# Performance work log

Hardware: AMD Instinct MI355X
Metric: run time of the kernel (lower is better)

The kernel has to match this reference:

```python
import jax, jax.numpy as jnp
import numpy as np

N_HEADS = 16


def setup_inputs() -> dict:
    key = jax.random.key(0)
    k1, k2, k3 = jax.random.split(key, 3)
    B, T, C = 4, 2048, 1024
    x = jax.random.normal(k1, (B, T, C), dtype=jnp.float32)
    # torch nn.Linear weights are (out_features, in_features); y = x @ W.T
    w_in = jax.random.normal(k2, (3 * C, C), dtype=jnp.float32) * 0.02
    w_out = jax.random.normal(k3, (C, C), dtype=jnp.float32) * 0.02
    return {"x": x, "w_in": w_in, "w_out": w_out}


def reference(x, w_in, w_out):
    B, T, C = x.shape
    H = N_HEADS
    hd = C // H

    qkv = x @ w_in.T                      # [B, T, 3C]
    q, k, v = jnp.split(qkv, 3, axis=2)   # each [B, T, C]

    def heads(t):
        return t.reshape(B, T, H, hd).transpose(0, 2, 1, 3)  # [B, H, T, hd]

    q, k, v = heads(q), heads(k), heads(v)

    scale = 1.0 / jnp.sqrt(jnp.float32(hd))
    scores = jnp.einsum('bhqd,bhkd->bhqk', q, k) * scale      # [B, H, T, T]
    causal = jnp.tril(jnp.ones((T, T), dtype=bool))
    scores = jnp.where(causal, scores, -jnp.inf)
    attn = jax.nn.softmax(scores, axis=-1)
    y = jnp.einsum('bhqk,bhkd->bhqd', attn, v)                # [B, H, T, hd]
    y = y.transpose(0, 2, 1, 3).reshape(B, T, C)
    return y @ w_out.T
```

## Files before the change

### kernel.cpp

```cpp
#include <hip/hip_runtime.h>
#include <stdint.h>

#define BB 4
#define TT 2048
#define CC 1024
#define HH 16
#define HD 64
#define C3 3072
#define MM (BB*TT)

typedef __bf16 bf16_t;
typedef bf16_t bf16x8 __attribute__((ext_vector_type(8)));
typedef float f32x4 __attribute__((ext_vector_type(4)));
typedef unsigned short u16;
typedef u16 u16x8 __attribute__((ext_vector_type(8)));
typedef uint32_t u32;

static __device__ __forceinline__ u16 f2bf(float f){
  u32 u = __builtin_bit_cast(u32, f);
  u32 r = (u + 0x7fffu + ((u >> 16) & 1u)) >> 16;
  return (u16)r;
}

static __device__ __forceinline__ f32x4 mfma16(bf16x8 a, bf16x8 b, f32x4 c){
  return __builtin_amdgcn_mfma_f32_16x16x32_bf16(a, b, c, 0, 0, 0);
}

typedef __attribute__((address_space(1))) void* gas_t;
typedef __attribute__((address_space(3))) void* las_t;
static __device__ __forceinline__ void gload16(const void* g, void* l){
  __builtin_amdgcn_global_load_lds((gas_t)g, (las_t)l, 16, 0, 0);
}

__global__ __launch_bounds__(256) void cvt_bf16(const float* __restrict__ in,
                                                u16* __restrict__ out, int n8){
  int stride = gridDim.x * blockDim.x;
  for (int i = blockIdx.x * blockDim.x + threadIdx.x; i < n8; i += stride){
    const float4* p = (const float4*)in + (size_t)i * 2;
    float4 a = p[0], b = p[1];
    u16x8 o;
    o[0]=f2bf(a.x); o[1]=f2bf(a.y); o[2]=f2bf(a.z); o[3]=f2bf(a.w);
    o[4]=f2bf(b.x); o[5]=f2bf(b.y); o[6]=f2bf(b.z); o[7]=f2bf(b.w);
    *((u16x8*)out + i) = o;
  }
}

template<int OUTBF>
__global__ __launch_bounds__(256) void gemm_bt(const u16* __restrict__ A,
                                               const u16* __restrict__ Bm,
                                               void* __restrict__ Cp,
                                               int M, int N, int K,
                                               int nbx, int cpx){
  __shared__ u16 As[128*64];
  __shared__ u16 Bs[128*64];
  const int bid = blockIdx.x;
  const int nb = (bid & 7) * cpx + (bid >> 3);
  const int by = nb / nbx, bx = nb - by * nbx;
  const int tid  = threadIdx.x;
  const int lane = tid & 63;
  const int w    = tid >> 6;
  const int m0   = by * 128;
  const int n0   = bx * 128;
  const int wm   = (w >> 1) * 64;
  const int wn   = (w & 1) * 64;
  const int lr   = lane & 15;
  const int lg4  = lane >> 4;

  f32x4 acc[4][4] = {};

  const int rq  = tid >> 3;
  const int c8s = ((tid & 7) ^ (rq & 7)) * 8;
  const u16* gA = A  + (size_t)(m0 + rq) * K + c8s;
  const u16* gB = Bm + (size_t)(n0 + rq) * K + c8s;
  char* lA = (char*)As + tid*16;
  char* lB = (char*)Bs + tid*16;

  for (int k0 = 0; k0 < K; k0 += 64){
    #pragma unroll
    for (int q = 0; q < 4; q++){
      gload16(gA + (size_t)(q*32)*K + k0, lA + q*4096);
      gload16(gB + (size_t)(q*32)*K + k0, lB + q*4096);
    }
    __syncthreads();
    #pragma unroll
    for (int kk = 0; kk < 2; kk++){
      bf16x8 af[4], bfr[4];
      #pragma unroll
      for (int m = 0; m < 4; m++){
        int row = wm + m*16 + lr;
        int slot = ((kk<<2) | lg4) ^ (row & 7);
        af[m] = *(const bf16x8*)((const char*)As + row*128 + slot*16);
      }
      #pragma unroll
      for (int n = 0; n < 4; n++){
        int row = wn + n*16 + lr;
        int slot = ((kk<<2) | lg4) ^ (row & 7);
        bfr[n] = *(const bf16x8*)((const char*)Bs + row*128 + slot*16);
      }
      #pragma unroll
      for (int m = 0; m < 4; m++)
        #pragma unroll
        for (int n = 0; n < 4; n++)
          acc[m][n] = mfma16(af[m], bfr[n], acc[m][n]);
    }
    __syncthreads();
  }

  const int cr = lg4 * 4;
  #pragma unroll
  for (int m = 0; m < 4; m++)
    #pragma unroll
    for (int n = 0; n < 4; n++)
      #pragma unroll
      for (int j = 0; j < 4; j++){
        size_t row = (size_t)(m0 + wm + m*16 + cr + j);
        size_t col = (size_t)(n0 + wn + n*16 + lr);
        if (OUTBF) ((u16*)Cp)[row*(size_t)N + col] = f2bf(acc[m][n][j]);
        else       ((float*)Cp)[row*(size_t)N + col] = acc[m][n][j];
      }
}

__global__ __launch_bounds__(256, 3) void attn_fwd(const u16* __restrict__ qkv,
                                                   u16* __restrict__ y){
  __shared__ u16 Kl[64*72];
  __shared__ u16 Vt[64*72];
  const int bid = blockIdx.x;
  const int tq = bid >> 6;
  const int h = bid & 15, b = (bid >> 4) & 3;
  const int tid = threadIdx.x, lane = tid & 63, w = tid >> 6;
  const int lr = lane & 15, lg = lane >> 4;
  const size_t base = (size_t)b * TT * C3;
  const int qA = tq*64 + w*16;
  const int qB = (31-tq)*64 + w*16;
  const float SC = 0.18033688011112042f;

  bf16x8 qf[2][2];
  {
    const u16* qp0 = qkv + base + (size_t)(qA + lr) * C3 + h*HD;
    qf[0][0] = *(const bf16x8*)(qp0 + lg*8);
    qf[0][1] = *(const bf16x8*)(qp0 + 32 + lg*8);
    const u16* qp1 = qkv + base + (size_t)(qB + lr) * C3 + h*HD;
    qf[1][0] = *(const bf16x8*)(qp1 + lg*8);
    qf[1][1] = *(const bf16x8*)(qp1 + 32 + lg*8);
    #pragma unroll
    for (int m = 0; m < 2; m++)
      #pragma unroll
      for (int i = 0; i < 2; i++)
        #pragma unroll
        for (int e = 0; e < 8; e++)
          qf[m][i][e] = (bf16_t)((float)qf[m][i][e] * SC);
  }

  const int rK = tid >> 3, cK = tid & 7;
  const int rV = tid & 31, cV = tid >> 5;
  const u16* gK = qkv + base + (size_t)rK * C3 + CC   + h*HD + cK*8;
  const u16* gV = qkv + base + (size_t)rV * C3 + 2*CC + h*HD + cV*8;

  const int kkey = ((rK >> 3) & 1) << 5;
  const int kw0 = rK*72 + ((cK*8) ^ kkey);
  const int kw1 = (rK+32)*72 + ((cK*8) ^ kkey);

  const int rdx = ((lr >> 2) & 1) << 5;
  const int rbase = 8*(lr >> 2) + (lr & 3);

  u16x8 kreg[2], vreg[2];
  kreg[0] = *(const u16x8*)(gK);
  kreg[1] = *(const u16x8*)(gK + (size_t)32*C3);
  vreg[0] = *(const u16x8*)(gV);
  vreg[1] = *(const u16x8*)(gV + (size_t)32*C3);

  f32x4 o[2][4] = {};
  float mj[2] = {-1e30f, -1e30f};
  float lj[2] = {0.f, 0.f};

  const int ktmax = 31 - tq;
  for (int kt = 0; kt <= ktmax; kt++){
    __syncthreads();
    *(u16x8*)&Kl[kw0] = kreg[0];
    *(u16x8*)&Kl[kw1] = kreg[1];
    #pragma unroll
    for (int i = 0; i < 2; i++)
      #pragma unroll
      for (int e = 0; e < 8; e++)
        Vt[(cV*8+e)*72 + i*32 + rV] = vreg[i][e];
    __syncthreads();

    if (kt < ktmax){
      const u16* gk2 = gK + (size_t)(kt+1)*64*C3;
      const u16* gv2 = gV + (size_t)(kt+1)*64*C3;
      kreg[0] = *(const u16x8*)(gk2);
      kreg[1] = *(const u16x8*)(gk2 + (size_t)32*C3);
      vreg[0] = *(const u16x8*)(gv2);
      vreg[1] = *(const u16x8*)(gv2 + (size_t)32*C3);
    }

    const bool m0act = (kt <= tq);

    f32x4 s[2][4] = {};
    __builtin_amdgcn_s_setprio(1);
    #pragma unroll
    for (int n = 0; n < 4; n++){
      const int rho = 32*(n>>1) + 4*(n&1) + rbase;
      bf16x8 kb0 = *(const bf16x8*)&Kl[rho*72 + ((     lg*8) ^ rdx)];
      bf16x8 kb1 = *(const bf16x8*)&Kl[rho*72 + ((32 + lg*8) ^ rdx)];
      if (m0act){
        s[0][n] = mfma16(kb0, qf[0][0], s[0][n]);
        s[0][n] = mfma16(kb1, qf[0][1], s[0][n]);
      }
      s[1][n] = mfma16(kb0, qf[1][0], s[1][n]);
      s[1][n] = mfma16(kb1, qf[1][1], s[1][n]);
    }
    __builtin_amdgcn_s_setprio(0);

    bf16x8 paA[2], paB[2];
    #pragma unroll
    for (int m = 0; m < 2; m++){
      if (m == 0 && !m0act) continue;
      const int qrow = (m ? qB : qA) + lr;
      const bool dm = (kt == (m ? ktmax : tq));
      if (dm){
        #pragma unroll
        for (int n = 0; n < 4; n++)
          #pragma unroll
          for (int j = 0; j < 4; j++)
            if (kt*64 + 32*(n>>1) + 8*lg + 4*(n&1) + j > qrow)
              s[m][n][j] = -1e30f;
      }
      float tm = s[m][0][0];
      #pragma unroll
      for (int n = 0; n < 4; n++)
        #pragma unroll
        for (int j = 0; j < 4; j++) tm = fmaxf(tm, s[m][n][j]);
      tm = fmaxf(tm, __shfl_xor(tm, 16, 64));
      tm = fmaxf(tm, __shfl_xor(tm, 32, 64));
      float mo = mj[m];
      if (!__all(tm <= mo + 4.0f)){
        float mn = fmaxf(mo, tm);
        float al = __builtin_amdgcn_exp2f(mo - mn);
        mj[m] = mn;
        lj[m] *= al;
        float a0 = __shfl(al, lg*4+0, 16);
        float a1 = __shfl(al, lg*4+1, 16);
        float a2 = __shfl(al, lg*4+2, 16);
        float a3 = __shfl(al, lg*4+3, 16);
        #pragma unroll
        for (int n = 0; n < 4; n++){
          o[m][n][0] *= a0; o[m][n][1] *= a1;
          o[m][n][2] *= a2; o[m][n][3] *= a3;
        }
      }
      float mm = mj[m];
      float ps = 0.f;
      bf16x8 pa, pb;
      #pragma unroll
      for (int n = 0; n < 4; n++){
        float p0 = __builtin_amdgcn_exp2f(s[m][n][0] - mm);
        float p1 = __builtin_amdgcn_exp2f(s[m][n][1] - mm);
        float p2 = __builtin_amdgcn_exp2f(s[m][n][2] - mm);
        float p3 = __builtin_amdgcn_exp2f(s[m][n][3] - mm);
        ps += (p0 + p1) + (p2 + p3);
        if (n == 0){ pa[0]=(bf16_t)p0; pa[1]=(bf16_t)p1; pa[2]=(bf16_t)p2; pa[3]=(bf16_t)p3; }
        if (n == 1){ pa[4]=(bf16_t)p0; pa[5]=(bf16_t)p1; pa[6]=(bf16_t)p2; pa[7]=(bf16_t)p3; }
        if (n == 2){ pb[0]=(bf16_t)p0; pb[1]=(bf16_t)p1; pb[2]=(bf16_t)p2; pb[3]=(bf16_t)p3; }
        if (n == 3){ pb[4]=(bf16_t)p0; pb[5]=(bf16_t)p1; pb[6]=(bf16_t)p2; pb[7]=(bf16_t)p3; }
      }
      ps += __shfl_xor(ps, 16, 64);
      ps += __shfl_xor(ps, 32, 64);
      lj[m] += ps;
      paA[m] = pa; paB[m] = pb;
    }

    __builtin_amdgcn_s_setprio(1);
    #pragma unroll
    for (int n = 0; n < 4; n++){
      bf16x8 vb0 = *(const bf16x8*)&Vt[(n*16+lr)*72 +      lg*8];
      bf16x8 vb1 = *(const bf16x8*)&Vt[(n*16+lr)*72 + 32 + lg*8];
      if (m0act){
        o[0][n] = mfma16(paA[0], vb0, o[0][n]);
        o[0][n] = mfma16(paB[0], vb1, o[0][n]);
      }
      o[1][n] = mfma16(paA[1], vb0, o[1][n]);
      o[1][n] = mfma16(paB[1], vb1, o[1][n]);
    }
    __builtin_amdgcn_s_setprio(0);
  }

  #pragma unroll
  for (int m = 0; m < 2; m++){
    float inv = 1.0f / lj[m];
    float i0 = __shfl(inv, lg*4+0, 16);
    float i1 = __shfl(inv, lg*4+1, 16);
    float i2 = __shfl(inv, lg*4+2, 16);
    float i3 = __shfl(inv, lg*4+3, 16);
    const int qb = (m ? qB : qA);
    #pragma unroll
    for (int j = 0; j < 4; j++){
      float ij = (j==0) ? i0 : (j==1) ? i1 : (j==2) ? i2 : i3;
      size_t row = (size_t)b*TT + qb + lg*4 + j;
      #pragma unroll
      for (int n = 0; n < 4; n++)
        y[row*CC + h*HD + n*16 + lr] = f2bf(o[m][n][j] * ij);
    }
  }
}

extern "C" void kernel_launch(void* const* d_in, const int* in_sizes, int n_in,
                              void* d_out, int out_size, void* d_ws, size_t ws_size,
                              hipStream_t stream){
  const float* x     = (const float*)d_in[0];
  const float* w_in  = (const float*)d_in[1];
  const float* w_out = (const float*)d_in[2];
  float* out = (float*)d_out;

  u16* xb   = (u16*)d_ws;
  u16* wib  = xb  + (size_t)MM * CC;
  u16* wob  = wib + (size_t)C3 * CC;
  u16* qkvb = wob + (size_t)CC * CC;
  u16* yb   = xb;

  auto nblk = [](int n8){ int g = (n8 + 255) / 256; return g > 2048 ? 2048 : g; };
  cvt_bf16<<<nblk(MM*CC/8), 256, 0, stream>>>(x,     xb,  MM*CC/8);
  cvt_bf16<<<nblk(C3*CC/8), 256, 0, stream>>>(w_in,  wib, C3*CC/8);
  cvt_bf16<<<nblk(CC*CC/8), 256, 0, stream>>>(w_out, wob, CC*CC/8);

  gemm_bt<1><<<1536, 256, 0, stream>>>(xb, wib, (void*)qkvb, MM, C3, CC, 24, 192);
  attn_fwd<<<1024, 256, 0, stream>>>(qkvb, yb);
  gemm_bt<0><<<512, 256, 0, stream>>>(yb, wob, (void*)out, MM, CC, CC, 8, 64);
}
```

Before: 172.7 us.

## Double-buffer K/V LDS tiles and pack V transpose stores into 32-bit writes

Shared-memory K and V tiles are now double-buffered by iteration parity, so the leading __syncthreads per iteration is dropped and only one barrier per key tile remains. The V transpose is remapped so each thread loads two adjacent key rows and writes packed pairs of bf16 as 32-bit LDS stores, halving the number of scalar LDS writes. This doubles LDS usage per block, which may affect occupancy at 3 blocks/CU, and changes the global V load pattern.

```diff
diff --git a/kernel.cpp b/kernel.cpp
--- a/kernel.cpp
+++ b/kernel.cpp
@@ -122,8 +122,8 @@
 
 __global__ __launch_bounds__(256, 3) void attn_fwd(const u16* __restrict__ qkv,
                                                    u16* __restrict__ y){
-  __shared__ u16 Kl[64*72];
-  __shared__ u16 Vt[64*72];
+  __shared__ u16 Kl[2][64*72];
+  __shared__ u16 Vt[2][64*72];
   const int bid = blockIdx.x;
   const int tq = bid >> 6;
   const int h = bid & 15, b = (bid >> 4) & 3;
@@ -152,13 +152,16 @@
   }
 
   const int rK = tid >> 3, cK = tid & 7;
-  const int rV = tid & 31, cV = tid >> 5;
-  const u16* gK = qkv + base + (size_t)rK * C3 + CC   + h*HD + cK*8;
-  const u16* gV = qkv + base + (size_t)rV * C3 + 2*CC + h*HD + cV*8;
+  const int rp = tid & 15;
+  const int dc = (tid >> 4) & 7;
+  const int hf = tid >> 7;
+  const u16* gK = qkv + base + (size_t)rK * C3 + CC + h*HD + cK*8;
+  const u16* gV = qkv + base + (size_t)(2*rp + 32*hf) * C3 + 2*CC + h*HD + dc*8;
 
   const int kkey = ((rK >> 3) & 1) << 5;
   const int kw0 = rK*72 + ((cK*8) ^ kkey);
   const int kw1 = (rK+32)*72 + ((cK*8) ^ kkey);
+  const int vw  = 2*rp + 32*hf;
 
   const int rdx = ((lr >> 2) & 1) << 5;
   const int rbase = 8*(lr >> 2) + (lr & 3);
@@ -167,7 +170,7 @@
   kreg[0] = *(const u16x8*)(gK);
   kreg[1] = *(const u16x8*)(gK + (size_t)32*C3);
   vreg[0] = *(const u16x8*)(gV);
-  vreg[1] = *(const u16x8*)(gV + (size_t)32*C3);
+  vreg[1] = *(const u16x8*)(gV + C3);
 
   f32x4 o[2][4] = {};
   float mj[2] = {-1e30f, -1e30f};
@@ -175,14 +178,16 @@
 
   const int ktmax = 31 - tq;
   for (int kt = 0; kt <= ktmax; kt++){
-    __syncthreads();
-    *(u16x8*)&Kl[kw0] = kreg[0];
-    *(u16x8*)&Kl[kw1] = kreg[1];
-    #pragma unroll
-    for (int i = 0; i < 2; i++)
-      #pragma unroll
-      for (int e = 0; e < 8; e++)
-        Vt[(cV*8+e)*72 + i*32 + rV] = vreg[i][e];
+    const int cb = kt & 1;
+    u16* KL = Kl[cb];
+    u16* VT = Vt[cb];
+    *(u16x8*)&KL[kw0] = kreg[0];
+    *(u16x8*)&KL[kw1] = kreg[1];
+    #pragma unroll
+    for (int e = 0; e < 8; e++){
+      u32 pk = (u32)vreg[0][e] | ((u32)vreg[1][e] << 16);
+      *(u32*)&VT[(dc*8+e)*72 + vw] = pk;
+    }
     __syncthreads();
 
     if (kt < ktmax){
@@ -191,7 +196,7 @@
       kreg[0] = *(const u16x8*)(gk2);
       kreg[1] = *(const u16x8*)(gk2 + (size_t)32*C3);
       vreg[0] = *(const u16x8*)(gv2);
-      vreg[1] = *(const u16x8*)(gv2 + (size_t)32*C3);
+      vreg[1] = *(const u16x8*)(gv2 + C3);
     }
 
     const bool m0act = (kt <= tq);
@@ -201,8 +206,8 @@
     #pragma unroll
     for (int n = 0; n < 4; n++){
       const int rho = 32*(n>>1) + 4*(n&1) + rbase;
-      bf16x8 kb0 = *(const bf16x8*)&Kl[rho*72 + ((     lg*8) ^ rdx)];
-      bf16x8 kb1 = *(const bf16x8*)&Kl[rho*72 + ((32 + lg*8) ^ rdx)];
+      bf16x8 kb0 = *(const bf16x8*)&KL[rho*72 + ((     lg*8) ^ rdx)];
+      bf16x8 kb1 = *(const bf16x8*)&KL[rho*72 + ((32 + lg*8) ^ rdx)];
       if (m0act){
         s[0][n] = mfma16(kb0, qf[0][0], s[0][n]);
         s[0][n] = mfma16(kb1, qf[0][1], s[0][n]);
@@ -273,8 +278,8 @@
     __builtin_amdgcn_s_setprio(1);
     #pragma unroll
     for (int n = 0; n < 4; n++){
-      bf16x8 vb0 = *(const bf16x8*)&Vt[(n*16+lr)*72 +      lg*8];
-      bf16x8 vb1 = *(const bf16x8*)&Vt[(n*16+lr)*72 + 32 + lg*8];
+      bf16x8 vb0 = *(const bf16x8*)&VT[(n*16+lr)*72 +      lg*8];
+      bf16x8 vb1 = *(const bf16x8*)&VT[(n*16+lr)*72 + 32 + lg*8];
       if (m0act){
         o[0][n] = mfma16(paA[0], vb0, o[0][n]);
         o[0][n] = mfma16(paB[0], vb1, o[0][n]);
```

Result: no change. 172.4 us (-0.2%).
